# Kernel optimization log

Measured on AMD Instinct MI355X. Metric: run time of the kernel, lower is better.

The kernel has to match this reference:

```python
import jax, jax.numpy as jnp
import numpy as np

# Production-scale dims: N tokens = 64 batch x 8192 seq, hidden width 256.
N, D_IN, D_OUT = 524288, 256, 256
P_NONZERO = 0.05  # mimics bnn.random.calc_desired_var -> sparse ternary W


def binarise(v):
    # bnn.functions.binarise forward: sign with binarise(0) = +1
    return jnp.where(v >= 0, 1.0, -1.0).astype(v.dtype)


def setup_inputs() -> dict:
    key = jax.random.key(0)
    kx, kw = jax.random.split(key)
    # x: binary activations in {-1,+1} (output of a previous binarise layer)
    x = jnp.where(jax.random.normal(kx, (N, D_IN)) >= 0, 1.0, -1.0).astype(jnp.float32)
    # W: ternary {-1, 0, +1} with Var = P_NONZERO (values +-1 each w.p. p/2)
    u = jax.random.uniform(kw, (D_IN, D_OUT))
    W = jnp.where(u < P_NONZERO / 2, -1.0,
                  jnp.where(u < P_NONZERO, 1.0, 0.0)).astype(jnp.float32)
    return {"x": x, "W": W}


def reference(x, W):
    # integer = x @ W  (ternary-weight matmul; int math in torch, same values in fp32)
    integer = x @ W  # [N, D_OUT]
    return binarise(integer)
```

## Files before the change

### kernel.cpp

```cpp
#include <hip/hip_runtime.h>
#include <stdint.h>


#define NROWS 524288
#define DDIM  256
#define BLOCKS 2048
#define ROWS_PER_BLOCK (NROWS / BLOCKS)
#define ITERS (ROWS_PER_BLOCK / 4)

typedef uint32_t u32;
typedef unsigned long long u64;

__global__ __launch_bounds__(256, 4)
void ternbin_kernel(const float* __restrict__ x, const float* __restrict__ W,
                    float* __restrict__ out) {
    const int t    = threadIdx.x;
    const int lane = t & 63;
    const int wv   = t >> 6;
    const int col  = (wv << 6) | lane;

    u32 A[8] = {0,0,0,0,0,0,0,0};
    u32 M[8] = {0,0,0,0,0,0,0,0};
    #pragma unroll 8
    for (int k = 0; k < DDIM; ++k) {
        const float v = W[k * DDIM + col];
        const int   w = ((k & 3) << 1) | (k >> 7);
        const u32 bit = 1u << ((k >> 2) & 31);
        if (v != 0.0f) A[w] |= bit;
        if (v <  0.0f) M[w] |= bit;
    }
    int C = 0;
    #pragma unroll
    for (int w = 0; w < 8; ++w) C += __popc(A[w]);

    const size_t row0 = (size_t)blockIdx.x * ROWS_PER_BLOCK;
    const float* xp = x   + row0 * DDIM + 4 * lane;
    float*       op = out + row0 * DDIM + col;

    #pragma unroll 1
    for (int it = 0; it < ITERS; ++it) {
        const int rbase = it << 2;
        uint4 xv[4];
        #pragma unroll
        for (int rr = 0; rr < 4; ++rr)
            xv[rr] = *reinterpret_cast<const uint4*>(xp + (size_t)(rbase + rr) * DDIM);

        #pragma unroll
        for (int rr = 0; rr < 4; ++rr) {
            const u64 b0 = __ballot((int)xv[rr].x < 0);
            const u64 b1 = __ballot((int)xv[rr].y < 0);
            const u64 b2 = __ballot((int)xv[rr].z < 0);
            const u64 b3 = __ballot((int)xv[rr].w < 0);
            const u32 s0 = (u32)b0, s1 = (u32)(b0 >> 32);
            const u32 s2 = (u32)b1, s3 = (u32)(b1 >> 32);
            const u32 s4 = (u32)b2, s5 = (u32)(b2 >> 32);
            const u32 s6 = (u32)b3, s7 = (u32)(b3 >> 32);

            int p = 0;
            p += __popc((s0 ^ M[0]) & A[0]);
            p += __popc((s1 ^ M[1]) & A[1]);
            p += __popc((s2 ^ M[2]) & A[2]);
            p += __popc((s3 ^ M[3]) & A[3]);
            p += __popc((s4 ^ M[4]) & A[4]);
            p += __popc((s5 ^ M[5]) & A[5]);
            p += __popc((s6 ^ M[6]) & A[6]);
            p += __popc((s7 ^ M[7]) & A[7]);
            const int d = C - 2 * p;
            const u32 o = 0x3f800000u | ((u32)d & 0x80000000u);
            __builtin_nontemporal_store(o,
                reinterpret_cast<u32*>(op + (size_t)(rbase + rr) * DDIM));
        }
    }
}

extern "C" void kernel_launch(void* const* d_in, const int* in_sizes, int n_in,
                              void* d_out, int out_size, void* d_ws, size_t ws_size,
                              hipStream_t stream) {
    const float* x = (const float*)d_in[0];
    const float* W = (const float*)d_in[1];
    float* out = (float*)d_out;
    ternbin_kernel<<<BLOCKS, 256, 0, stream>>>(x, W, out);
}
```

Measured before the change: 936.6 us.

## Double-buffer x row loads with software pipelining and sched barriers

```diff
diff --git a/kernel.cpp b/kernel.cpp
--- a/kernel.cpp
+++ b/kernel.cpp
@@ -6,10 +6,41 @@
 #define DDIM  256
 #define BLOCKS 2048
 #define ROWS_PER_BLOCK (NROWS / BLOCKS)
-#define ITERS (ROWS_PER_BLOCK / 4)
 
 typedef uint32_t u32;
 typedef unsigned long long u64;
+
+#define LOADG(v0, v1, v2, v3, ptr)                                   \
+    v0 = *reinterpret_cast<const uint4*>(ptr);                       \
+    v1 = *reinterpret_cast<const uint4*>((ptr) + DDIM);              \
+    v2 = *reinterpret_cast<const uint4*>((ptr) + 2 * DDIM);          \
+    v3 = *reinterpret_cast<const uint4*>((ptr) + 3 * DDIM);
+
+#define PROC1(xv, optr)                                               \
+    {                                                                 \
+        const u64 _bl0 = __ballot((int)(xv).x < 0);                   \
+        const u64 _bl1 = __ballot((int)(xv).y < 0);                   \
+        const u64 _bl2 = __ballot((int)(xv).z < 0);                   \
+        const u64 _bl3 = __ballot((int)(xv).w < 0);                   \
+        int _p = 0;                                                   \
+        _p += __popc(((u32)_bl0         ^ M0) & A0);                  \
+        _p += __popc(((u32)(_bl0 >> 32) ^ M1) & A1);                  \
+        _p += __popc(((u32)_bl1         ^ M2) & A2);                  \
+        _p += __popc(((u32)(_bl1 >> 32) ^ M3) & A3);                  \
+        _p += __popc(((u32)_bl2         ^ M4) & A4);                  \
+        _p += __popc(((u32)(_bl2 >> 32) ^ M5) & A5);                  \
+        _p += __popc(((u32)_bl3         ^ M6) & A6);                  \
+        _p += __popc(((u32)(_bl3 >> 32) ^ M7) & A7);                  \
+        const int _d = C - 2 * _p;                                    \
+        const u32 _o = 0x3f800000u | ((u32)_d & 0x80000000u);         \
+        __builtin_nontemporal_store(_o, reinterpret_cast<u32*>(optr));\
+    }
+
+#define PROC4(v0, v1, v2, v3, optr)                                  \
+    PROC1(v0, (optr));                                               \
+    PROC1(v1, (optr) + DDIM);                                        \
+    PROC1(v2, (optr) + 2 * DDIM);                                    \
+    PROC1(v3, (optr) + 3 * DDIM);
 
 __global__ __launch_bounds__(256, 4)
 void ternbin_kernel(const float* __restrict__ x, const float* __restrict__ W,
@@ -19,58 +50,49 @@
     const int wv   = t >> 6;
     const int col  = (wv << 6) | lane;
 
-    u32 A[8] = {0,0,0,0,0,0,0,0};
-    u32 M[8] = {0,0,0,0,0,0,0,0};
+    u32 A0=0,A1=0,A2=0,A3=0,A4=0,A5=0,A6=0,A7=0;
+    u32 M0=0,M1=0,M2=0,M3=0,M4=0,M5=0,M6=0,M7=0;
     #pragma unroll 8
     for (int k = 0; k < DDIM; ++k) {
         const float v = W[k * DDIM + col];
         const int   w = ((k & 3) << 1) | (k >> 7);
         const u32 bit = 1u << ((k >> 2) & 31);
-        if (v != 0.0f) A[w] |= bit;
-        if (v <  0.0f) M[w] |= bit;
+        const u32 nz  = (v != 0.0f) ? bit : 0u;
+        const u32 ng  = (v <  0.0f) ? bit : 0u;
+        switch (w) {
+            case 0: A0 |= nz; M0 |= ng; break;
+            case 1: A1 |= nz; M1 |= ng; break;
+            case 2: A2 |= nz; M2 |= ng; break;
+            case 3: A3 |= nz; M3 |= ng; break;
+            case 4: A4 |= nz; M4 |= ng; break;
+            case 5: A5 |= nz; M5 |= ng; break;
+            case 6: A6 |= nz; M6 |= ng; break;
+            case 7: A7 |= nz; M7 |= ng; break;
+        }
     }
-    int C = 0;
-    #pragma unroll
-    for (int w = 0; w < 8; ++w) C += __popc(A[w]);
+    const int C = __popc(A0) + __popc(A1) + __popc(A2) + __popc(A3)
+                + __popc(A4) + __popc(A5) + __popc(A6) + __popc(A7);
 
     const size_t row0 = (size_t)blockIdx.x * ROWS_PER_BLOCK;
-    const float* xp = x   + row0 * DDIM + 4 * lane;
-    float*       op = out + row0 * DDIM + col;
+    const float* xq = x   + row0 * DDIM + 4 * lane;
+    float*       oq = out + row0 * DDIM + col;
+
+    uint4 a0, a1, a2, a3, b0, b1, b2, b3;
+    LOADG(a0, a1, a2, a3, xq); xq += 4 * DDIM;
+    LOADG(b0, b1, b2, b3, xq); xq += 4 * DDIM;
+    __builtin_amdgcn_sched_barrier(0);
 
     #pragma unroll 1
-    for (int it = 0; it < ITERS; ++it) {
-        const int rbase = it << 2;
-        uint4 xv[4];
-        #pragma unroll
-        for (int rr = 0; rr < 4; ++rr)
-            xv[rr] = *reinterpret_cast<const uint4*>(xp + (size_t)(rbase + rr) * DDIM);
-
-        #pragma unroll
-        for (int rr = 0; rr < 4; ++rr) {
-            const u64 b0 = __ballot((int)xv[rr].x < 0);
-            const u64 b1 = __ballot((int)xv[rr].y < 0);
-            const u64 b2 = __ballot((int)xv[rr].z < 0);
-            const u64 b3 = __ballot((int)xv[rr].w < 0);
-            const u32 s0 = (u32)b0, s1 = (u32)(b0 >> 32);
-            const u32 s2 = (u32)b1, s3 = (u32)(b1 >> 32);
-            const u32 s4 = (u32)b2, s5 = (u32)(b2 >> 32);
-            const u32 s6 = (u32)b3, s7 = (u32)(b3 >> 32);
-
-            int p = 0;
-            p += __popc((s0 ^ M[0]) & A[0]);
-            p += __popc((s1 ^ M[1]) & A[1]);
-            p += __popc((s2 ^ M[2]) & A[2]);
-            p += __popc((s3 ^ M[3]) & A[3]);
-            p += __popc((s4 ^ M[4]) & A[4]);
-            p += __popc((s5 ^ M[5]) & A[5]);
-            p += __popc((s6 ^ M[6]) & A[6]);
-            p += __popc((s7 ^ M[7]) & A[7]);
-            const int d = C - 2 * p;
-            const u32 o = 0x3f800000u | ((u32)d & 0x80000000u);
-            __builtin_nontemporal_store(o,
-                reinterpret_cast<u32*>(op + (size_t)(rbase + rr) * DDIM));
-        }
+    for (int k = 0; k < 31; ++k) {
+        PROC4(a0, a1, a2, a3, oq); oq += 4 * DDIM;
+        LOADG(a0, a1, a2, a3, xq); xq += 4 * DDIM;
+        __builtin_amdgcn_sched_barrier(0);
+        PROC4(b0, b1, b2, b3, oq); oq += 4 * DDIM;
+        LOADG(b0, b1, b2, b3, xq); xq += 4 * DDIM;
+        __builtin_amdgcn_sched_barrier(0);
     }
+    PROC4(a0, a1, a2, a3, oq); oq += 4 * DDIM;
+    PROC4(b0, b1, b2, b3, oq);
 }
 
 extern "C" void kernel_launch(void* const* d_in, const int* in_sizes, int n_in,
```

Measured after the change: 1.039 ms. 11.0% more time.
